# Optimization experiments

Measured on AMD Instinct MI355X. Metric: run time of the kernel, lower is better.

Reference implementation:

```python
import jax, jax.numpy as jnp
import numpy as np

C_MSA, C_Z, C_HID, N_HEADS = 64, 128, 32, 8
INF = 1e8
EPS = 1e-5

def layer_norm(x, g, b):
    mu = jnp.mean(x, axis=-1, keepdims=True)
    var = jnp.var(x, axis=-1, keepdims=True)
    return (x - mu) * jax.lax.rsqrt(var + EPS) * g + b

def setup_inputs() -> dict:
    key = jax.random.key(0)
    ks = jax.random.split(key, 8)
    n_seq, n_res = 256, 512
    m = jax.random.normal(ks[0], (n_seq, n_res, C_MSA), dtype=jnp.float32)
    z = jax.random.normal(ks[1], (n_res, n_res, C_Z), dtype=jnp.float32)
    msa_mask = jnp.ones((n_seq, n_res), dtype=jnp.float32)
    z_mask = jnp.ones((n_res, n_res), dtype=jnp.float32)
    hc = N_HEADS * C_HID
    s_v = 1.0 / np.sqrt(C_MSA)
    W_v = jax.random.normal(ks[2], (hc, C_MSA), dtype=jnp.float32) * s_v
    W_g = jax.random.normal(ks[3], (hc, C_MSA), dtype=jnp.float32) * s_v  # 'gating' init is zeros; random for testing
    W_b = jax.random.normal(ks[4], (N_HEADS, C_Z), dtype=jnp.float32) * (1.0 / np.sqrt(C_Z))
    W_o = jax.random.normal(ks[5], (C_MSA, hc), dtype=jnp.float32) * (1.0 / np.sqrt(hc))
    ln_m_g = jnp.ones((C_MSA,), jnp.float32); ln_m_b = jnp.zeros((C_MSA,), jnp.float32)
    ln_z_g = jnp.ones((C_Z,), jnp.float32); ln_z_b = jnp.zeros((C_Z,), jnp.float32)
    return {"m": m, "z": z, "msa_mask": msa_mask, "z_mask": z_mask,
            "ln_m_g": ln_m_g, "ln_m_b": ln_m_b, "W_v": W_v, "W_g": W_g,
            "ln_z_g": ln_z_g, "ln_z_b": ln_z_b, "W_b": W_b, "W_o": W_o}

def reference(m, z, msa_mask, z_mask, ln_m_g, ln_m_b, W_v, W_g, ln_z_g, ln_z_b, W_b, W_o):
    n_seq, n_res, _ = m.shape
    m_ln = layer_norm(m, ln_m_g, ln_m_b)                      # [s, i, c_msa]
    v = (m_ln @ W_v.T).reshape(n_seq, n_res, N_HEADS, C_HID)  # [s, j, h, c]
    g = jax.nn.sigmoid(m_ln @ W_g.T).reshape(n_seq, n_res, N_HEADS, C_HID)
    b = layer_norm(z, ln_z_g, ln_z_b) @ W_b.T                 # [i, j, h]
    b = b + INF * (z_mask[..., None] - 1.0)
    v = v * msa_mask[..., None, None]
    w = jax.nn.softmax(b, axis=-2)                            # softmax over j
    # o[s,i,h,c] = sum_j v[s,j,h,c] * w[i,j,h]  (no broadcast materialization)
    o = g * jnp.einsum('sjhc,ijh->sihc', v, w)
    out = o.reshape(n_seq, n_res, N_HEADS * C_HID) @ W_o.T    # [s, i, c_msa]
    return out
```

## Files before the change

### kernel.cpp

```cpp
#include <hip/hip_runtime.h>
#include <stdint.h>


typedef unsigned short u16;
typedef unsigned int u32;
typedef __attribute__((ext_vector_type(4))) float f32x4;
typedef __attribute__((ext_vector_type(8))) short bf16x8;

__device__ __forceinline__ u16 f2bf(float f) {
  u32 u = __float_as_uint(f);
  u = u + 0x7fffu + ((u >> 16) & 1u);
  return (u16)(u >> 16);
}
__device__ __forceinline__ float bf2f(u16 h) { return __uint_as_float(((u32)h) << 16); }

__device__ __forceinline__ bf16x8 pack8(const float* f) {
  bf16x8 r;
#pragma unroll
  for (int e = 0; e < 8; ++e) r[e] = (short)f2bf(f[e]);
  return r;
}

#define GLD_LDS16(gp, lp) __builtin_amdgcn_global_load_lds(                 \
    (__attribute__((address_space(1))) const void*)(gp),                    \
    (__attribute__((address_space(3))) void*)(lp), 16, 0, 0)

__global__ __launch_bounds__(256) void k0_convert(
    const float* __restrict__ W_v, const float* __restrict__ W_g,
    const float* __restrict__ W_o, const float* __restrict__ W_b,
    u16* __restrict__ Wvg, u16* __restrict__ Wo, u16* __restrict__ Wb)
{
  int id = blockIdx.x * 256 + threadIdx.x;
  if (id < 32768) {
    int row = id >> 6, col = id & 63;
    float v = (row < 256) ? W_v[row * 64 + col] : W_g[(row - 256) * 64 + col];
    Wvg[id] = f2bf(v);
  } else if (id < 49152) {
    int k = id - 32768;
    Wo[k] = f2bf(W_o[k]);
  } else if (id < 51200) {
    int k = id - 49152;
    Wb[k] = (k < 1024) ? f2bf(W_b[k]) : (u16)0;
  }
}

__global__ __launch_bounds__(256) void k1a_bias(
    const float* __restrict__ z, const float* __restrict__ z_mask,
    const float* __restrict__ gzp, const float* __restrict__ bzp,
    const u16* __restrict__ Wb, float* __restrict__ bbuf)
{
  const int jc = blockIdx.x, i = blockIdx.y;
  const int j0 = jc * 128;
  const int t = threadIdx.x, lane = t & 63, wid = t >> 6;
  const int r16 = lane & 15, kg = lane >> 4;
  __shared__ char zns[32768];
  __shared__ float bl[8][132];
  __shared__ float gz[128], bz[128];
  if (t < 128) { gz[t] = gzp[t]; bz[t] = bzp[t]; }
  __syncthreads();

#pragma unroll
  for (int rr = 0; rr < 2; ++rr) {
    const int row = rr * 64 + (t >> 2), part = t & 3;
    const float* zr = z + ((size_t)i * 512 + j0 + row) * 128 + part * 32;
    f32x4 v[8];
    float s = 0.f, sq = 0.f;
#pragma unroll
    for (int q = 0; q < 8; ++q) {
      v[q] = *reinterpret_cast<const f32x4*>(zr + 4 * q);
#pragma unroll
      for (int e = 0; e < 4; ++e) { s += v[q][e]; sq += v[q][e] * v[q][e]; }
    }
    s += __shfl_xor(s, 1); s += __shfl_xor(s, 2);
    sq += __shfl_xor(sq, 1); sq += __shfl_xor(sq, 2);
    float mean = s * (1.f / 128.f);
    float rstd = rsqrtf(sq * (1.f / 128.f) - mean * mean + 1e-5f);
#pragma unroll
    for (int uu = 0; uu < 4; ++uu) {
      float tmp[8];
#pragma unroll
      for (int e = 0; e < 8; ++e) {
        int k = part * 32 + uu * 8 + e;
        tmp[e] = (v[uu * 2 + (e >> 2)][e & 3] - mean) * rstd * gz[k] + bz[k];
      }
      int byte = (row * 256 + part * 64 + uu * 16) ^ ((row & 7) << 4);
      *reinterpret_cast<bf16x8*>(zns + byte) = pack8(tmp);
    }
  }
  __syncthreads();

  bf16x8 av[2][4], bw[4];
#pragma unroll
  for (int mf = 0; mf < 2; ++mf)
#pragma unroll
    for (int kf = 0; kf < 4; ++kf) {
      int row = wid * 32 + mf * 16 + r16;
      int byte = (row * 256 + (kf * 4 + kg) * 16) ^ ((row & 7) << 4);
      av[mf][kf] = *reinterpret_cast<const bf16x8*>(zns + byte);
    }
#pragma unroll
  for (int kf = 0; kf < 4; ++kf)
    bw[kf] = *reinterpret_cast<const bf16x8*>(Wb + r16 * 128 + kf * 32 + kg * 8);
  f32x4 acc[2];
  acc[0] = (f32x4){0.f, 0.f, 0.f, 0.f}; acc[1] = acc[0];
#pragma unroll
  for (int mf = 0; mf < 2; ++mf)
#pragma unroll
    for (int kf = 0; kf < 4; ++kf)
      acc[mf] = __builtin_amdgcn_mfma_f32_16x16x32_bf16(av[mf][kf], bw[kf], acc[mf], 0, 0, 0);
  if (r16 < 8) {
#pragma unroll
    for (int mf = 0; mf < 2; ++mf)
#pragma unroll
      for (int r = 0; r < 4; ++r)
        bl[r16][wid * 32 + mf * 16 + kg * 4 + r] = acc[mf][r];
  }
  __syncthreads();

  {
    const int h = t >> 5, jj = t & 31;
    f32x4 bv = *reinterpret_cast<const f32x4*>(&bl[h][jj * 4]);
    f32x4 zm = *reinterpret_cast<const f32x4*>(z_mask + (size_t)i * 512 + j0 + jj * 4);
#pragma unroll
    for (int e = 0; e < 4; ++e) bv[e] += 1e8f * (zm[e] - 1.f);
    *reinterpret_cast<f32x4*>(bbuf + ((size_t)h * 512 + i) * 512 + j0 + jj * 4) = bv;
  }
}

__global__ __launch_bounds__(256) void k1b_softmax(
    const float* __restrict__ bbuf, u16* __restrict__ wbuf)
{
  const int t = threadIdx.x, lane = t & 63, wid = t >> 6;
  const size_t row = (size_t)blockIdx.x * 4 + wid;
  const float* src = bbuf + row * 512 + lane * 8;
  f32x4 a = *reinterpret_cast<const f32x4*>(src);
  f32x4 b = *reinterpret_cast<const f32x4*>(src + 4);
  float vals[8];
#pragma unroll
  for (int e = 0; e < 4; ++e) { vals[e] = a[e]; vals[4 + e] = b[e]; }
  float mx = vals[0];
#pragma unroll
  for (int e = 1; e < 8; ++e) mx = fmaxf(mx, vals[e]);
#pragma unroll
  for (int m = 1; m < 64; m <<= 1) mx = fmaxf(mx, __shfl_xor(mx, m));
  float sum = 0.f;
#pragma unroll
  for (int e = 0; e < 8; ++e) { vals[e] = __expf(vals[e] - mx); sum += vals[e]; }
#pragma unroll
  for (int m = 1; m < 64; m <<= 1) sum += __shfl_xor(sum, m);
  float inv = 1.f / sum;
  bf16x8 o;
#pragma unroll
  for (int e = 0; e < 8; ++e) o[e] = (short)f2bf(vals[e] * inv);
  *reinterpret_cast<bf16x8*>(wbuf + row * 512 + lane * 8) = o;
}

__global__ __launch_bounds__(512) void k2_vg(
    const float* __restrict__ m, const float* __restrict__ msa_mask,
    const float* __restrict__ gmp, const float* __restrict__ bmp,
    const u16* __restrict__ Wvg, u16* __restrict__ vT, u16* __restrict__ gbuf)
{
  const int jt = blockIdx.x, s = blockIdx.y;
  const int j0 = jt * 128;
  const int t = threadIdx.x, lane = t & 63, wid = t >> 6;
  const int r16 = lane & 15, kg = lane >> 4;
  __shared__ char smem[65536];
  __shared__ float maskl[128], gk[64], bk[64];
  if (t < 64) gk[t] = gmp[t];
  else if (t < 128) bk[t - 64] = bmp[t - 64];
  if (t < 128) maskl[t] = msa_mask[(size_t)s * 512 + j0 + t];
  __syncthreads();

  {
    const int row = t >> 2, part = t & 3;
    const float* mr = m + ((size_t)s * 512 + j0 + row) * 64 + part * 16;
    f32x4 v[4];
    float sm = 0.f, sq = 0.f;
#pragma unroll
    for (int q = 0; q < 4; ++q) {
      v[q] = *reinterpret_cast<const f32x4*>(mr + 4 * q);
#pragma unroll
      for (int e = 0; e < 4; ++e) { sm += v[q][e]; sq += v[q][e] * v[q][e]; }
    }
    sm += __shfl_xor(sm, 1); sm += __shfl_xor(sm, 2);
    sq += __shfl_xor(sq, 1); sq += __shfl_xor(sq, 2);
    float mean = sm * (1.f / 64.f);
    float rstd = rsqrtf(sq * (1.f / 64.f) - mean * mean + 1e-5f);
#pragma unroll
    for (int uu = 0; uu < 2; ++uu) {
      float tmp[8];
#pragma unroll
      for (int e = 0; e < 8; ++e) {
        int k = part * 16 + uu * 8 + e;
        tmp[e] = (v[uu * 2 + (e >> 2)][e & 3] - mean) * rstd * gk[k] + bk[k];
      }
      int byte = (row * 128 + part * 32 + uu * 16) ^ ((row & 7) << 4);
      *reinterpret_cast<bf16x8*>(smem + byte) = pack8(tmp);
    }
  }
  __syncthreads();

  const int jh = wid & 1, hcq0 = wid >> 1;
  bf16x8 av[4][2];
#pragma unroll
  for (int mf = 0; mf < 4; ++mf)
#pragma unroll
    for (int kf = 0; kf < 2; ++kf) {
      int row = jh * 64 + mf * 16 + r16;
      int byte = (row * 128 + (kf * 4 + kg) * 16) ^ ((row & 7) << 4);
      av[mf][kf] = *reinterpret_cast<const bf16x8*>(smem + byte);
    }
  __syncthreads();

#pragma unroll
  for (int rep = 0; rep < 2; ++rep) {
    const int hcq = hcq0 + rep * 4;
    bf16x8 bv[4][2];
#pragma unroll
    for (int nf = 0; nf < 4; ++nf)
#pragma unroll
      for (int kf = 0; kf < 2; ++kf)
        bv[nf][kf] = *reinterpret_cast<const bf16x8*>(
            Wvg + (hcq * 64 + nf * 16 + r16) * 64 + kf * 32 + kg * 8);
    f32x4 acc[4][4];
#pragma unroll
    for (int mf = 0; mf < 4; ++mf)
#pragma unroll
      for (int nf = 0; nf < 4; ++nf) acc[mf][nf] = (f32x4){0.f, 0.f, 0.f, 0.f};
#pragma unroll
    for (int mf = 0; mf < 4; ++mf)
#pragma unroll
      for (int nf = 0; nf < 4; ++nf)
#pragma unroll
        for (int kf = 0; kf < 2; ++kf)
          acc[mf][nf] = __builtin_amdgcn_mfma_f32_16x16x32_bf16(av[mf][kf], bv[nf][kf], acc[mf][nf], 0, 0, 0);

    if (rep == 0) {
#pragma unroll
      for (int mf = 0; mf < 4; ++mf)
#pragma unroll
        for (int nf = 0; nf < 4; ++nf)
#pragma unroll
          for (int r = 0; r < 4; ++r) {
            int j = jh * 64 + mf * 16 + kg * 4 + r;
            int hc = hcq * 64 + nf * 16 + r16;
            float val = acc[mf][nf][r] * maskl[j];
            int byte = (hc * 256 + j * 2) ^ ((hc & 7) << 4);
            *reinterpret_cast<u16*>(smem + byte) = f2bf(val);
          }
      __syncthreads();
#pragma unroll
      for (int it = 0; it < 8; ++it) {
        int u = it * 512 + t;
        int hc = u >> 4, sub = u & 15;
        int byte = (hc * 256 + sub * 16) ^ ((hc & 7) << 4);
        bf16x8 rv = *reinterpret_cast<const bf16x8*>(smem + byte);
        int h = hc >> 5, c = hc & 31;
        *reinterpret_cast<bf16x8*>(
            vT + (((size_t)h * 8192 + s * 32 + c) * 512 + j0 + sub * 8)) = rv;
      }
    } else {
#pragma unroll
      for (int mf = 0; mf < 4; ++mf)
#pragma unroll
        for (int nf = 0; nf < 4; ++nf)
#pragma unroll
          for (int r = 0; r < 4; ++r) {
            int j = jh * 64 + mf * 16 + kg * 4 + r;
            int hc = hcq0 * 64 + nf * 16 + r16;
            float val = 1.f / (1.f + __expf(-acc[mf][nf][r]));
            gbuf[((size_t)s * 512 + j0 + j) * 256 + hc] = f2bf(val);
          }
    }
  }
}

__global__ __launch_bounds__(256) void k3_einsum(
    const u16* __restrict__ wbuf, const u16* __restrict__ vT, u16* __restrict__ O2)
{
  const int nt = blockIdx.x, mt = blockIdx.y, h = blockIdx.z;
  const int t = threadIdx.x, lane = t & 63, wid = t >> 6;
  const int Mbase = mt * 128, Nbase = nt * 128;
  __shared__ char smem[32768];
  const u16* Ag = wbuf + (size_t)h * 262144;
  const u16* Bg = vT + (size_t)h * 4194304;
  const int wr = wid >> 1, wc = wid & 1;
  const int r16 = lane & 15, kg = lane >> 4;
  const int lrow = lane >> 3, lslot = lane & 7;
  f32x4 acc[4][4];
#pragma unroll
  for (int a = 0; a < 4; ++a)
#pragma unroll
    for (int b = 0; b < 4; ++b) acc[a][b] = (f32x4){0.f, 0.f, 0.f, 0.f};

  for (int kt = 0; kt < 8; ++kt) {
    const int k0 = kt * 64;
#pragma unroll
    for (int q = 0; q < 4; ++q) {
      const int rb = wid * 32 + q * 8;
      const int pr = rb + lrow;
      const int su = (lslot ^ (pr & 7)) * 8;
      GLD_LDS16(Ag + (size_t)(Mbase + pr) * 512 + k0 + su, (u16*)smem + rb * 64);
      GLD_LDS16(Bg + (size_t)(Nbase + pr) * 512 + k0 + su, (u16*)(smem + 16384) + rb * 64);
    }
    __syncthreads();
    bf16x8 av[4][2], bv[4][2];
#pragma unroll
    for (int mf = 0; mf < 4; ++mf)
#pragma unroll
      for (int kf = 0; kf < 2; ++kf) {
        int rowA = wr * 64 + mf * 16 + r16;
        int byteA = (rowA * 128 + (kf * 4 + kg) * 16) ^ ((rowA & 7) << 4);
        av[mf][kf] = *reinterpret_cast<const bf16x8*>(smem + byteA);
        int rowB = wc * 64 + mf * 16 + r16;
        int byteB = (rowB * 128 + (kf * 4 + kg) * 16) ^ ((rowB & 7) << 4);
        bv[mf][kf] = *reinterpret_cast<const bf16x8*>(smem + 16384 + byteB);
      }
#pragma unroll
    for (int mf = 0; mf < 4; ++mf)
#pragma unroll
      for (int nf = 0; nf < 4; ++nf)
#pragma unroll
        for (int kf = 0; kf < 2; ++kf)
          acc[mf][nf] = __builtin_amdgcn_mfma_f32_16x16x32_bf16(av[mf][kf], bv[nf][kf], acc[mf][nf], 0, 0, 0);
    __syncthreads();
  }

  u16* Tep = (u16*)smem;
#pragma unroll
  for (int mf = 0; mf < 4; ++mf)
#pragma unroll
    for (int nf = 0; nf < 4; ++nf)
#pragma unroll
      for (int r = 0; r < 4; ++r) {
        int il = wr * 64 + mf * 16 + kg * 4 + r;
        int sc = wc * 64 + nf * 16 + r16;
        Tep[il * 128 + sc] = f2bf(acc[mf][nf][r]);
      }
  __syncthreads();
#pragma unroll
  for (int it = 0; it < 8; ++it) {
    int u = it * 256 + t;
    int il = u >> 4, sub = u & 15;
    bf16x8 rv = *reinterpret_cast<const bf16x8*>(Tep + il * 128 + sub * 8);
    int scg = Nbase + sub * 8;
    int sI = scg >> 5, c = scg & 31;
    *reinterpret_cast<bf16x8*>(
        O2 + (((size_t)(Mbase + il) * 256 + sI) * 256 + h * 32 + c)) = rv;
  }
}

__global__ __launch_bounds__(256) void k4_out(
    const u16* __restrict__ O2, const u16* __restrict__ gbuf,
    const u16* __restrict__ Wo, float* __restrict__ out)
{
  const int st = blockIdx.x, i = blockIdx.y;
  const int s0 = st * 64;
  const int t = threadIdx.x, lane = t & 63, wid = t >> 6;
  const int r16 = lane & 15, kg = lane >> 4;
  __shared__ u16 Al[64][264];
  __shared__ u16 Wl[64][264];
#pragma unroll
  for (int it = 0; it < 8; ++it) {
    int u = it * 256 + t, row = u >> 5, sub = u & 31;
    *reinterpret_cast<bf16x8*>(&Wl[row][sub * 8]) =
        *reinterpret_cast<const bf16x8*>(Wo + row * 256 + sub * 8);
  }
  {
    const int sl = t >> 2, hc0 = (t & 3) * 64;
    const u16* Op = O2 + ((size_t)i * 256 + s0 + sl) * 256 + hc0;
    const u16* gp = gbuf + ((size_t)(s0 + sl) * 512 + i) * 256 + hc0;
#pragma unroll
    for (int uu = 0; uu < 8; ++uu) {
      bf16x8 ov = *reinterpret_cast<const bf16x8*>(Op + uu * 8);
      bf16x8 gv = *reinterpret_cast<const bf16x8*>(gp + uu * 8);
      bf16x8 r;
#pragma unroll
      for (int e = 0; e < 8; ++e) r[e] = (short)f2bf(bf2f((u16)ov[e]) * bf2f((u16)gv[e]));
      *reinterpret_cast<bf16x8*>(&Al[sl][hc0 + uu * 8]) = r;
    }
  }
  __syncthreads();

  f32x4 acc[4];
#pragma unroll
  for (int nf = 0; nf < 4; ++nf) acc[nf] = (f32x4){0.f, 0.f, 0.f, 0.f};
#pragma unroll
  for (int kf = 0; kf < 8; ++kf) {
    bf16x8 a = *reinterpret_cast<const bf16x8*>(&Al[wid * 16 + r16][kf * 32 + kg * 8]);
#pragma unroll
    for (int nf = 0; nf < 4; ++nf) {
      bf16x8 b = *reinterpret_cast<const bf16x8*>(&Wl[nf * 16 + r16][kf * 32 + kg * 8]);
      acc[nf] = __builtin_amdgcn_mfma_f32_16x16x32_bf16(a, b, acc[nf], 0, 0, 0);
    }
  }
#pragma unroll
  for (int nf = 0; nf < 4; ++nf)
#pragma unroll
    for (int r = 0; r < 4; ++r)
      out[((size_t)(s0 + wid * 16 + kg * 4 + r) * 512 + i) * 64 + nf * 16 + r16] = acc[nf][r];
}

extern "C" void kernel_launch(void* const* d_in, const int* in_sizes, int n_in,
                              void* d_out, int out_size, void* d_ws, size_t ws_size,
                              hipStream_t stream) {
  const float* m        = (const float*)d_in[0];
  const float* z        = (const float*)d_in[1];
  const float* msa_mask = (const float*)d_in[2];
  const float* z_mask   = (const float*)d_in[3];
  const float* ln_m_g   = (const float*)d_in[4];
  const float* ln_m_b   = (const float*)d_in[5];
  const float* W_v      = (const float*)d_in[6];
  const float* W_g      = (const float*)d_in[7];
  const float* ln_z_g   = (const float*)d_in[8];
  const float* ln_z_b   = (const float*)d_in[9];
  const float* W_b      = (const float*)d_in[10];
  const float* W_o      = (const float*)d_in[11];
  float* out = (float*)d_out;

  char* ws = (char*)d_ws;
  u16*   Wvg  = (u16*)(ws);
  u16*   Wo   = (u16*)(ws + 65536);
  u16*   Wb   = (u16*)(ws + 98304);
  float* bbuf = (float*)(ws + (1u  << 20));
  u16*   wbuf = (u16*)  (ws + (9u  << 20));
  u16*   vT   = (u16*)  (ws + (16u << 20));
  u16*   gbuf = (u16*)  (ws + (80u << 20));
  u16*   O2   = (u16*)  (ws + (144u << 20));

  k0_convert<<<200, 256, 0, stream>>>(W_v, W_g, W_o, W_b, Wvg, Wo, Wb);
  k1a_bias<<<dim3(4, 512), 256, 0, stream>>>(z, z_mask, ln_z_g, ln_z_b, Wb, bbuf);
  k1b_softmax<<<1024, 256, 0, stream>>>(bbuf, wbuf);
  k2_vg<<<dim3(4, 256), 512, 0, stream>>>(m, msa_mask, ln_m_g, ln_m_b, Wvg, vT, gbuf);
  k3_einsum<<<dim3(64, 4, 8), 256, 0, stream>>>(wbuf, vT, O2);
  k4_out<<<dim3(4, 512), 256, 0, stream>>>(O2, gbuf, Wo, out);
}
```

Before: 379.8 us.

## Fuse bias and softmax kernels, restructure vg stores and coalesce output writes

Merges the pair-bias kernel and the softmax kernel into one block per row i, so the fp32 bias buffer no longer round-trips through global memory. In k2, v is now written straight from registers with packed stores, and the gate is staged through LDS for coalesced stores. k3 linearizes the grid so that heads are interleaved across blocks. k4 stages its output tile in LDS so it can write coalesced f32x4 rows. The fused k1 has only 512 blocks, each looping serially over four j chunks, which lowers parallelism in that stage.

```diff
diff --git a/kernel.cpp b/kernel.cpp
--- a/kernel.cpp
+++ b/kernel.cpp
@@ -44,115 +44,111 @@
   }
 }
 
-__global__ __launch_bounds__(256) void k1a_bias(
+__global__ __launch_bounds__(256) void k1_fused(
     const float* __restrict__ z, const float* __restrict__ z_mask,
     const float* __restrict__ gzp, const float* __restrict__ bzp,
-    const u16* __restrict__ Wb, float* __restrict__ bbuf)
+    const u16* __restrict__ Wb, u16* __restrict__ wbuf)
 {
-  const int jc = blockIdx.x, i = blockIdx.y;
-  const int j0 = jc * 128;
+  const int i = blockIdx.x;
   const int t = threadIdx.x, lane = t & 63, wid = t >> 6;
   const int r16 = lane & 15, kg = lane >> 4;
   __shared__ char zns[32768];
-  __shared__ float bl[8][132];
+  __shared__ float bbl[8][520];
   __shared__ float gz[128], bz[128];
   if (t < 128) { gz[t] = gzp[t]; bz[t] = bzp[t]; }
-  __syncthreads();
-
-#pragma unroll
-  for (int rr = 0; rr < 2; ++rr) {
-    const int row = rr * 64 + (t >> 2), part = t & 3;
-    const float* zr = z + ((size_t)i * 512 + j0 + row) * 128 + part * 32;
-    f32x4 v[8];
-    float s = 0.f, sq = 0.f;
-#pragma unroll
-    for (int q = 0; q < 8; ++q) {
-      v[q] = *reinterpret_cast<const f32x4*>(zr + 4 * q);
-#pragma unroll
-      for (int e = 0; e < 4; ++e) { s += v[q][e]; sq += v[q][e] * v[q][e]; }
-    }
-    s += __shfl_xor(s, 1); s += __shfl_xor(s, 2);
-    sq += __shfl_xor(sq, 1); sq += __shfl_xor(sq, 2);
-    float mean = s * (1.f / 128.f);
-    float rstd = rsqrtf(sq * (1.f / 128.f) - mean * mean + 1e-5f);
-#pragma unroll
-    for (int uu = 0; uu < 4; ++uu) {
-      float tmp[8];
-#pragma unroll
-      for (int e = 0; e < 8; ++e) {
-        int k = part * 32 + uu * 8 + e;
-        tmp[e] = (v[uu * 2 + (e >> 2)][e & 3] - mean) * rstd * gz[k] + bz[k];
-      }
-      int byte = (row * 256 + part * 64 + uu * 16) ^ ((row & 7) << 4);
-      *reinterpret_cast<bf16x8*>(zns + byte) = pack8(tmp);
-    }
-  }
-  __syncthreads();
-
-  bf16x8 av[2][4], bw[4];
-#pragma unroll
-  for (int mf = 0; mf < 2; ++mf)
-#pragma unroll
-    for (int kf = 0; kf < 4; ++kf) {
-      int row = wid * 32 + mf * 16 + r16;
-      int byte = (row * 256 + (kf * 4 + kg) * 16) ^ ((row & 7) << 4);
-      av[mf][kf] = *reinterpret_cast<const bf16x8*>(zns + byte);
-    }
+  bf16x8 bw[4];
 #pragma unroll
   for (int kf = 0; kf < 4; ++kf)
     bw[kf] = *reinterpret_cast<const bf16x8*>(Wb + r16 * 128 + kf * 32 + kg * 8);
-  f32x4 acc[2];
-  acc[0] = (f32x4){0.f, 0.f, 0.f, 0.f}; acc[1] = acc[0];
-#pragma unroll
-  for (int mf = 0; mf < 2; ++mf)
-#pragma unroll
-    for (int kf = 0; kf < 4; ++kf)
-      acc[mf] = __builtin_amdgcn_mfma_f32_16x16x32_bf16(av[mf][kf], bw[kf], acc[mf], 0, 0, 0);
-  if (r16 < 8) {
+  __syncthreads();
+
+  for (int jc = 0; jc < 4; ++jc) {
+    const int j0 = jc * 128;
+#pragma unroll
+    for (int rr = 0; rr < 2; ++rr) {
+      const int row = rr * 64 + (t >> 2), part = t & 3;
+      const float* zr = z + ((size_t)i * 512 + j0 + row) * 128 + part * 32;
+      f32x4 v[8];
+      float s = 0.f, sq = 0.f;
+#pragma unroll
+      for (int q = 0; q < 8; ++q) {
+        v[q] = *reinterpret_cast<const f32x4*>(zr + 4 * q);
+#pragma unroll
+        for (int e = 0; e < 4; ++e) { s += v[q][e]; sq += v[q][e] * v[q][e]; }
+      }
+      s += __shfl_xor(s, 1); s += __shfl_xor(s, 2);
+      sq += __shfl_xor(sq, 1); sq += __shfl_xor(sq, 2);
+      float mean = s * (1.f / 128.f);
+      float rstd = rsqrtf(sq * (1.f / 128.f) - mean * mean + 1e-5f);
+#pragma unroll
+      for (int uu = 0; uu < 4; ++uu) {
+        float tmp[8];
+#pragma unroll
+        for (int e = 0; e < 8; ++e) {
+          int k = part * 32 + uu * 8 + e;
+          tmp[e] = (v[uu * 2 + (e >> 2)][e & 3] - mean) * rstd * gz[k] + bz[k];
+        }
+        int byte = (row * 256 + part * 64 + uu * 16) ^ ((row & 7) << 4);
+        *reinterpret_cast<bf16x8*>(zns + byte) = pack8(tmp);
+      }
+    }
+    __syncthreads();
+
+    bf16x8 av[2][4];
 #pragma unroll
     for (int mf = 0; mf < 2; ++mf)
 #pragma unroll
-      for (int r = 0; r < 4; ++r)
-        bl[r16][wid * 32 + mf * 16 + kg * 4 + r] = acc[mf][r];
-  }
-  __syncthreads();
-
-  {
-    const int h = t >> 5, jj = t & 31;
-    f32x4 bv = *reinterpret_cast<const f32x4*>(&bl[h][jj * 4]);
-    f32x4 zm = *reinterpret_cast<const f32x4*>(z_mask + (size_t)i * 512 + j0 + jj * 4);
-#pragma unroll
-    for (int e = 0; e < 4; ++e) bv[e] += 1e8f * (zm[e] - 1.f);
-    *reinterpret_cast<f32x4*>(bbuf + ((size_t)h * 512 + i) * 512 + j0 + jj * 4) = bv;
-  }
-}
-
-__global__ __launch_bounds__(256) void k1b_softmax(
-    const float* __restrict__ bbuf, u16* __restrict__ wbuf)
-{
-  const int t = threadIdx.x, lane = t & 63, wid = t >> 6;
-  const size_t row = (size_t)blockIdx.x * 4 + wid;
-  const float* src = bbuf + row * 512 + lane * 8;
-  f32x4 a = *reinterpret_cast<const f32x4*>(src);
-  f32x4 b = *reinterpret_cast<const f32x4*>(src + 4);
-  float vals[8];
-#pragma unroll
-  for (int e = 0; e < 4; ++e) { vals[e] = a[e]; vals[4 + e] = b[e]; }
-  float mx = vals[0];
-#pragma unroll
-  for (int e = 1; e < 8; ++e) mx = fmaxf(mx, vals[e]);
-#pragma unroll
-  for (int m = 1; m < 64; m <<= 1) mx = fmaxf(mx, __shfl_xor(mx, m));
-  float sum = 0.f;
-#pragma unroll
-  for (int e = 0; e < 8; ++e) { vals[e] = __expf(vals[e] - mx); sum += vals[e]; }
-#pragma unroll
-  for (int m = 1; m < 64; m <<= 1) sum += __shfl_xor(sum, m);
-  float inv = 1.f / sum;
-  bf16x8 o;
-#pragma unroll
-  for (int e = 0; e < 8; ++e) o[e] = (short)f2bf(vals[e] * inv);
-  *reinterpret_cast<bf16x8*>(wbuf + row * 512 + lane * 8) = o;
+      for (int kf = 0; kf < 4; ++kf) {
+        int row = wid * 32 + mf * 16 + r16;
+        int byte = (row * 256 + (kf * 4 + kg) * 16) ^ ((row & 7) << 4);
+        av[mf][kf] = *reinterpret_cast<const bf16x8*>(zns + byte);
+      }
+    f32x4 acc[2];
+    acc[0] = (f32x4){0.f, 0.f, 0.f, 0.f}; acc[1] = acc[0];
+#pragma unroll
+    for (int mf = 0; mf < 2; ++mf)
+#pragma unroll
+      for (int kf = 0; kf < 4; ++kf)
+        acc[mf] = __builtin_amdgcn_mfma_f32_16x16x32_bf16(av[mf][kf], bw[kf], acc[mf], 0, 0, 0);
+    if (r16 < 8) {
+#pragma unroll
+      for (int mf = 0; mf < 2; ++mf)
+#pragma unroll
+        for (int r = 0; r < 4; ++r)
+          bbl[r16][j0 + wid * 32 + mf * 16 + kg * 4 + r] = acc[mf][r];
+    }
+    __syncthreads();
+  }
+
+  f32x4 zm0 = *reinterpret_cast<const f32x4*>(z_mask + (size_t)i * 512 + lane * 8);
+  f32x4 zm1 = *reinterpret_cast<const f32x4*>(z_mask + (size_t)i * 512 + lane * 8 + 4);
+  float mbias[8];
+#pragma unroll
+  for (int e = 0; e < 4; ++e) { mbias[e] = 1e8f * (zm0[e] - 1.f); mbias[4 + e] = 1e8f * (zm1[e] - 1.f); }
+#pragma unroll
+  for (int hh = 0; hh < 2; ++hh) {
+    const int h = wid * 2 + hh;
+    f32x4 a = *reinterpret_cast<const f32x4*>(&bbl[h][lane * 8]);
+    f32x4 b = *reinterpret_cast<const f32x4*>(&bbl[h][lane * 8 + 4]);
+    float vals[8];
+#pragma unroll
+    for (int e = 0; e < 4; ++e) { vals[e] = a[e] + mbias[e]; vals[4 + e] = b[e] + mbias[4 + e]; }
+    float mx = vals[0];
+#pragma unroll
+    for (int e = 1; e < 8; ++e) mx = fmaxf(mx, vals[e]);
+#pragma unroll
+    for (int msk = 1; msk < 64; msk <<= 1) mx = fmaxf(mx, __shfl_xor(mx, msk));
+    float sum = 0.f;
+#pragma unroll
+    for (int e = 0; e < 8; ++e) { vals[e] = __expf(vals[e] - mx); sum += vals[e]; }
+#pragma unroll
+    for (int msk = 1; msk < 64; msk <<= 1) sum += __shfl_xor(sum, msk);
+    float inv = 1.f / sum;
+    bf16x8 o;
+#pragma unroll
+    for (int e = 0; e < 8; ++e) o[e] = (short)f2bf(vals[e] * inv);
+    *reinterpret_cast<bf16x8*>(wbuf + ((size_t)h * 512 + i) * 512 + lane * 8) = o;
+  }
 }
 
 __global__ __launch_bounds__(512) void k2_vg(
@@ -212,16 +208,14 @@
     }
   __syncthreads();
 
-#pragma unroll
-  for (int rep = 0; rep < 2; ++rep) {
-    const int hcq = hcq0 + rep * 4;
+  {
     bf16x8 bv[4][2];
 #pragma unroll
     for (int nf = 0; nf < 4; ++nf)
 #pragma unroll
       for (int kf = 0; kf < 2; ++kf)
         bv[nf][kf] = *reinterpret_cast<const bf16x8*>(
-            Wvg + (hcq * 64 + nf * 16 + r16) * 64 + kf * 32 + kg * 8);
+            Wvg + (hcq0 * 64 + nf * 16 + r16) * 64 + kf * 32 + kg * 8);
     f32x4 acc[4][4];
 #pragma unroll
     for (int mf = 0; mf < 4; ++mf)
@@ -234,51 +228,72 @@
 #pragma unroll
         for (int kf = 0; kf < 2; ++kf)
           acc[mf][nf] = __builtin_amdgcn_mfma_f32_16x16x32_bf16(av[mf][kf], bv[nf][kf], acc[mf][nf], 0, 0, 0);
-
-    if (rep == 0) {
-#pragma unroll
-      for (int mf = 0; mf < 4; ++mf)
-#pragma unroll
-        for (int nf = 0; nf < 4; ++nf)
-#pragma unroll
-          for (int r = 0; r < 4; ++r) {
-            int j = jh * 64 + mf * 16 + kg * 4 + r;
-            int hc = hcq * 64 + nf * 16 + r16;
-            float val = acc[mf][nf][r] * maskl[j];
-            int byte = (hc * 256 + j * 2) ^ ((hc & 7) << 4);
-            *reinterpret_cast<u16*>(smem + byte) = f2bf(val);
-          }
-      __syncthreads();
-#pragma unroll
-      for (int it = 0; it < 8; ++it) {
-        int u = it * 512 + t;
-        int hc = u >> 4, sub = u & 15;
-        int byte = (hc * 256 + sub * 16) ^ ((hc & 7) << 4);
-        bf16x8 rv = *reinterpret_cast<const bf16x8*>(smem + byte);
-        int h = hc >> 5, c = hc & 31;
-        *reinterpret_cast<bf16x8*>(
-            vT + (((size_t)h * 8192 + s * 32 + c) * 512 + j0 + sub * 8)) = rv;
-      }
-    } else {
-#pragma unroll
-      for (int mf = 0; mf < 4; ++mf)
-#pragma unroll
-        for (int nf = 0; nf < 4; ++nf)
-#pragma unroll
-          for (int r = 0; r < 4; ++r) {
-            int j = jh * 64 + mf * 16 + kg * 4 + r;
-            int hc = hcq0 * 64 + nf * 16 + r16;
-            float val = 1.f / (1.f + __expf(-acc[mf][nf][r]));
-            gbuf[((size_t)s * 512 + j0 + j) * 256 + hc] = f2bf(val);
-          }
-    }
+#pragma unroll
+    for (int mf = 0; mf < 4; ++mf) {
+      const int jb = jh * 64 + mf * 16 + kg * 4;
+      const float m0 = maskl[jb], m1 = maskl[jb + 1], m2 = maskl[jb + 2], m3 = maskl[jb + 3];
+#pragma unroll
+      for (int nf = 0; nf < 4; ++nf) {
+        const int hc = hcq0 * 64 + nf * 16 + r16;
+        const int h = hc >> 5, c = hc & 31;
+        u32 lo = (u32)f2bf(acc[mf][nf][0] * m0) | ((u32)f2bf(acc[mf][nf][1] * m1) << 16);
+        u32 hi = (u32)f2bf(acc[mf][nf][2] * m2) | ((u32)f2bf(acc[mf][nf][3] * m3) << 16);
+        uint2 pk; pk.x = lo; pk.y = hi;
+        *reinterpret_cast<uint2*>(vT + (((size_t)h * 8192 + s * 32 + c) * 512 + j0 + jb)) = pk;
+      }
+    }
+  }
+
+  {
+    bf16x8 bv[4][2];
+#pragma unroll
+    for (int nf = 0; nf < 4; ++nf)
+#pragma unroll
+      for (int kf = 0; kf < 2; ++kf)
+        bv[nf][kf] = *reinterpret_cast<const bf16x8*>(
+            Wvg + ((hcq0 + 4) * 64 + nf * 16 + r16) * 64 + kf * 32 + kg * 8);
+    f32x4 acc[4][4];
+#pragma unroll
+    for (int mf = 0; mf < 4; ++mf)
+#pragma unroll
+      for (int nf = 0; nf < 4; ++nf) acc[mf][nf] = (f32x4){0.f, 0.f, 0.f, 0.f};
+#pragma unroll
+    for (int mf = 0; mf < 4; ++mf)
+#pragma unroll
+      for (int nf = 0; nf < 4; ++nf)
+#pragma unroll
+        for (int kf = 0; kf < 2; ++kf)
+          acc[mf][nf] = __builtin_amdgcn_mfma_f32_16x16x32_bf16(av[mf][kf], bv[nf][kf], acc[mf][nf], 0, 0, 0);
+#pragma unroll
+    for (int mf = 0; mf < 4; ++mf)
+#pragma unroll
+      for (int nf = 0; nf < 4; ++nf)
+#pragma unroll
+        for (int r = 0; r < 4; ++r) {
+          int j = jh * 64 + mf * 16 + kg * 4 + r;
+          int hc = hcq0 * 64 + nf * 16 + r16;
+          float val = 1.f / (1.f + __expf(-acc[mf][nf][r]));
+          int byte = (j * 512 + hc * 2) ^ ((j & 7) << 4);
+          *reinterpret_cast<u16*>(smem + byte) = f2bf(val);
+        }
+  }
+  __syncthreads();
+#pragma unroll
+  for (int it = 0; it < 8; ++it) {
+    int u = it * 512 + t;
+    int j = u >> 5, sub = u & 31;
+    int byte = (j * 512 + sub * 16) ^ ((j & 7) << 4);
+    bf16x8 rv = *reinterpret_cast<const bf16x8*>(smem + byte);
+    *reinterpret_cast<bf16x8*>(gbuf + (((size_t)s * 512 + j0 + j) * 256 + sub * 8)) = rv;
   }
 }
 
 __global__ __launch_bounds__(256) void k3_einsum(
     const u16* __restrict__ wbuf, const u16* __restrict__ vT, u16* __restrict__ O2)
 {
-  const int nt = blockIdx.x, mt = blockIdx.y, h = blockIdx.z;
+  const int id = blockIdx.x;
+  const int h = id & 7, pos = id >> 3;
+  const int nt = pos >> 2, mt = pos & 3;
   const int t = threadIdx.x, lane = t & 63, wid = t >> 6;
   const int Mbase = mt * 128, Nbase = nt * 128;
   __shared__ char smem[32768];
@@ -394,11 +409,21 @@
       acc[nf] = __builtin_amdgcn_mfma_f32_16x16x32_bf16(a, b, acc[nf], 0, 0, 0);
     }
   }
+  __syncthreads();
+  float* Ot = (float*)&Al[0][0];
 #pragma unroll
   for (int nf = 0; nf < 4; ++nf)
 #pragma unroll
     for (int r = 0; r < 4; ++r)
-      out[((size_t)(s0 + wid * 16 + kg * 4 + r) * 512 + i) * 64 + nf * 16 + r16] = acc[nf][r];
+      Ot[(wid * 16 + kg * 4 + r) * 68 + nf * 16 + r16] = acc[nf][r];
+  __syncthreads();
+#pragma unroll
+  for (int it = 0; it < 4; ++it) {
+    int u = it * 256 + t;
+    int row = u >> 4, unit = u & 15;
+    f32x4 rv = *reinterpret_cast<const f32x4*>(Ot + row * 68 + unit * 4);
+    *reinterpret_cast<f32x4*>(out + (((size_t)(s0 + row) * 512 + i) * 64 + unit * 4)) = rv;
+  }
 }
 
 extern "C" void kernel_launch(void* const* d_in, const int* in_sizes, int n_in,
@@ -422,16 +447,14 @@
   u16*   Wvg  = (u16*)(ws);
   u16*   Wo   = (u16*)(ws + 65536);
   u16*   Wb   = (u16*)(ws + 98304);
-  float* bbuf = (float*)(ws + (1u  << 20));
-  u16*   wbuf = (u16*)  (ws + (9u  << 20));
-  u16*   vT   = (u16*)  (ws + (16u << 20));
-  u16*   gbuf = (u16*)  (ws + (80u << 20));
-  u16*   O2   = (u16*)  (ws + (144u << 20));
+  u16*   wbuf = (u16*)  (ws + (1u  << 20));
+  u16*   vT   = (u16*)  (ws + (8u  << 20));
+  u16*   gbuf = (u16*)  (ws + (72u << 20));
+  u16*   O2   = (u16*)  (ws + (136u << 20));
 
   k0_convert<<<200, 256, 0, stream>>>(W_v, W_g, W_o, W_b, Wvg, Wo, Wb);
-  k1a_bias<<<dim3(4, 512), 256, 0, stream>>>(z, z_mask, ln_z_g, ln_z_b, Wb, bbuf);
-  k1b_softmax<<<1024, 256, 0, stream>>>(bbuf, wbuf);
+  k1_fused<<<512, 256, 0, stream>>>(z, z_mask, ln_z_g, ln_z_b, Wb, wbuf);
   k2_vg<<<dim3(4, 256), 512, 0, stream>>>(m, msa_mask, ln_m_g, ln_m_b, Wvg, vT, gbuf);
-  k3_einsum<<<dim3(64, 4, 8), 256, 0, stream>>>(wbuf, vT, O2);
+  k3_einsum<<<2048, 256, 0, stream>>>(wbuf, vT, O2);
   k4_out<<<dim3(4, 512), 256, 0, stream>>>(O2, gbuf, Wo, out);
 }
```

Result: no change. 379.8 us (+0.0%).
